# Performance work log

Measured on AMD Instinct MI355X. Metric: run time of the kernel, lower is better.

Reference implementation:

```python
import jax, jax.numpy as jnp
import numpy as np

N, C, H, W = 2, 128, 64, 64
N_HEAD = 4
GROUPS = 16
EPS = 1e-5


def group_norm(x, scale, offset):
    # haiku GroupNorm, channels_first: normalize over (channels-in-group, h, w)
    n, c, h, w = x.shape
    xg = x.reshape(n, GROUPS, c // GROUPS, h, w)
    mu = xg.mean(axis=(2, 3, 4), keepdims=True)
    var = xg.var(axis=(2, 3, 4), keepdims=True)
    xg = (xg - mu) * jax.lax.rsqrt(var + EPS)
    return xg.reshape(n, c, h, w) * scale[None, :, None, None] + offset[None, :, None, None]


def setup_inputs() -> dict:
    key = jax.random.key(0)
    ks = jax.random.split(key, 4)
    inv_sqrt_c = 1.0 / np.sqrt(C).astype(np.float32)
    return {
        "x": jax.random.normal(ks[0], (N, C, H, W), dtype=jnp.float32),
        "w_qkv": jax.random.normal(ks[1], (C, 3 * C), dtype=jnp.float32) * inv_sqrt_c,
        "b_qkv": jnp.zeros((3 * C,), dtype=jnp.float32),
        "w_out": jax.random.normal(ks[2], (C, C), dtype=jnp.float32) * inv_sqrt_c,
        "b_out": jnp.zeros((C,), dtype=jnp.float32),
        "gn1_scale": jnp.ones((C,), dtype=jnp.float32),
        "gn1_offset": jnp.zeros((C,), dtype=jnp.float32),
        "gn2_scale": jnp.ones((C,), dtype=jnp.float32),
        "gn2_offset": jnp.zeros((C,), dtype=jnp.float32),
    }


def reference(x, w_qkv, b_qkv, w_out, b_out, gn1_scale, gn1_offset, gn2_scale, gn2_offset):
    n, c, h, w = x.shape
    dh = c // N_HEAD
    # GroupNorm (x is reassigned, so the residual uses the normalized x)
    xn = group_norm(x, gn1_scale, gn1_offset)
    # 1x1 conv qkv projection: [n, 3c, h, w]
    qkv = jnp.einsum('nchw,cd->ndhw', xn, w_qkv) + b_qkv[None, :, None, None]
    # [n, 3H, dh, hw] -> [n, 3H, hw, dh]
    qkv = jnp.swapaxes(qkv.reshape(n, N_HEAD * 3, dh, h * w), 2, 3)
    q, k, v = jnp.split(qkv, 3, axis=1)  # each [n, H, hw, dh]
    scale = dh ** (-0.25)
    # [n, H, hw, hw] attention matrix (the memory-bound core)
    att = jax.nn.softmax((q * scale) @ (jnp.swapaxes(k, 2, 3) * scale), axis=3)
    y = jnp.swapaxes(att @ v, 2, 3).reshape(n, c, h, w)
    # 1x1 conv out projection + GroupNorm + residual
    out = jnp.einsum('nchw,cd->ndhw', y, w_out) + b_out[None, :, None, None]
    return xn + group_norm(out, gn2_scale, gn2_offset)
```

## Files before the change

### kernel.cpp

```cpp
#include <hip/hip_runtime.h>
#include <hip/hip_bf16.h>
#include <math.h>

constexpr int cHW   = 4096;
constexpr int cC    = 128;
constexpr int cNH   = 4;
constexpr int cDH   = 32;
constexpr float cEPS = 1e-5f;
constexpr float cQS = 0.2550347805f;
constexpr int SPLIT = 4;

typedef short bh8  __attribute__((ext_vector_type(8)));
typedef float f4   __attribute__((ext_vector_type(4)));
typedef float f16a __attribute__((ext_vector_type(16)));

static __device__ __forceinline__ unsigned short f2bf(float f) {
  union { __hip_bfloat16 h; unsigned short u; } cv;
  cv.h = __float2bfloat16(f);
  return cv.u;
}
static __device__ __forceinline__ unsigned pack2bf(float a, float b) {
  return (unsigned)f2bf(a) | ((unsigned)f2bf(b) << 16);
}
static __device__ __forceinline__ unsigned pack_trunc(float a, float b) {
  unsigned ua = __builtin_bit_cast(unsigned, a);
  unsigned ub = __builtin_bit_cast(unsigned, b);
  return (ua >> 16) | (ub & 0xffff0000u);
}
static __device__ __forceinline__ float bflo(unsigned pk) {
  return __builtin_bit_cast(float, pk << 16);
}
static __device__ __forceinline__ float bfhi(unsigned pk) {
  return __builtin_bit_cast(float, pk & 0xffff0000u);
}
static __device__ __forceinline__ void plswap(unsigned& a, unsigned& b) {
#if __has_builtin(__builtin_amdgcn_permlane32_swap)
  typedef int v2i __attribute__((ext_vector_type(2)));
  v2i r = __builtin_amdgcn_permlane32_swap((int)a, (int)b, false, false);
  a = (unsigned)r[0]; b = (unsigned)r[1];
#else
  asm("v_permlane32_swap_b32 %0, %1" : "+v"(a), "+v"(b));
#endif
}
static __device__ __forceinline__ bh8 mk8(unsigned a, unsigned b, unsigned c, unsigned d) {
  union { unsigned u[4]; bh8 v; } t;
  t.u[0] = a; t.u[1] = b; t.u[2] = c; t.u[3] = d;
  return t.v;
}

__device__ __forceinline__ void block_reduce2(float& a, float& b, float* sbuf) {
  #pragma unroll
  for (int off = 32; off > 0; off >>= 1) {
    a += __shfl_down(a, off, 64);
    b += __shfl_down(b, off, 64);
  }
  int wave = threadIdx.x >> 6;
  int lane = threadIdx.x & 63;
  if (lane == 0) { sbuf[wave] = a; sbuf[4 + wave] = b; }
  __syncthreads();
  if (threadIdx.x == 0) {
    sbuf[8] = sbuf[0] + sbuf[1] + sbuf[2] + sbuf[3];
    sbuf[9] = sbuf[4] + sbuf[5] + sbuf[6] + sbuf[7];
  }
  __syncthreads();
  a = sbuf[8];
  b = sbuf[9];
}

__global__ __launch_bounds__(256)
void prep(const float* __restrict__ x, float* __restrict__ part,
          const float* __restrict__ wq, const float* __restrict__ wo,
          unsigned short* __restrict__ wqT, unsigned short* __restrict__ woT) {
  __shared__ float lds[32 * 133];
  int L = threadIdx.x;
  if (blockIdx.x < 256) {
    int ng = blockIdx.x >> 3, sl = blockIdx.x & 7;
    const float4* s4 = (const float4*)x;
    float s = 0.f, s2 = 0.f;
    #pragma unroll
    for (int i = 0; i < 4; i++) {
      int idx = i * 256 + L;
      int c = idx >> 7, tt = idx & 127;
      float4 v = s4[(size_t)(ng * 8 + c) * 1024 + sl * 128 + tt];
      s  += v.x + v.y + v.z + v.w;
      s2 += v.x*v.x + v.y*v.y + v.z*v.z + v.w*v.w;
    }
    block_reduce2(s, s2, lds);
    if (L == 0) { part[blockIdx.x * 2] = s; part[blockIdx.x * 2 + 1] = s2; }
  } else {
    int bx = blockIdx.x - 256;
    const float* src; unsigned short* dst; int W, d0;
    if (bx < 12) { src = wq; dst = wqT; W = 384; d0 = bx * 32; }
    else         { src = wo; dst = woT; W = 128; d0 = (bx - 12) * 32; }
    #pragma unroll
    for (int i = 0; i < 16; i++) {
      int c = i * 8 + (L >> 5), d = L & 31;
      lds[d * 133 + c] = src[(size_t)c * W + d0 + d];
    }
    __syncthreads();
    int d = L >> 3, ch = L & 7, c0 = ch * 16;
    unsigned pk[8];
    #pragma unroll
    for (int j = 0; j < 8; j++)
      pk[j] = pack2bf(lds[d * 133 + c0 + 2 * j], lds[d * 133 + c0 + 2 * j + 1]);
    uint4* d4 = (uint4*)(dst + (size_t)(d0 + d) * 128 + c0);
    d4[0] = make_uint4(pk[0], pk[1], pk[2], pk[3]);
    d4[1] = make_uint4(pk[4], pk[5], pk[6], pk[7]);
  }
}

__global__ __launch_bounds__(256)
void gn_stats(const float* __restrict__ src, float* __restrict__ part) {
  __shared__ float sbuf[10];
  int ng = blockIdx.x >> 3, sl = blockIdx.x & 7;
  const float4* s4 = (const float4*)src;
  float s = 0.f, s2 = 0.f;
  #pragma unroll
  for (int i = 0; i < 4; i++) {
    int idx = i * 256 + threadIdx.x;
    int c = idx >> 7, tt = idx & 127;
    float4 v = s4[(size_t)(ng * 8 + c) * 1024 + sl * 128 + tt];
    s  += v.x + v.y + v.z + v.w;
    s2 += v.x*v.x + v.y*v.y + v.z*v.z + v.w*v.w;
  }
  block_reduce2(s, s2, sbuf);
  if (threadIdx.x == 0) { part[blockIdx.x * 2] = s; part[blockIdx.x * 2 + 1] = s2; }
}

__global__ __launch_bounds__(256)
void gn1_pack(const float* __restrict__ x, const float* __restrict__ part,
              const float* __restrict__ sc, const float* __restrict__ of,
              unsigned short* __restrict__ xnB) {
  int cc = blockIdx.x, ts = blockIdx.y, n = blockIdx.z;
  int ng = n * 16 + cc;
  float s = 0.f, s2 = 0.f;
  #pragma unroll
  for (int p = 0; p < 8; p++) { s += part[(ng*8+p)*2]; s2 += part[(ng*8+p)*2+1]; }
  float mu = s * (1.0f / 32768.0f);
  float rinv = rsqrtf(s2 * (1.0f / 32768.0f) - mu * mu + cEPS);
  int t = ts * 256 + threadIdx.x;
  float v[8];
  #pragma unroll
  for (int j = 0; j < 8; j++) {
    int c = cc * 8 + j;
    float a = rinv * sc[c];
    float bo = of[c] - mu * a;
    v[j] = x[((size_t)n * cC + c) * cHW + t] * a + bo;
  }
  unsigned pk[4];
  #pragma unroll
  for (int j = 0; j < 4; j++) pk[j] = pack2bf(v[2*j], v[2*j+1]);
  ((uint4*)xnB)[(size_t)(n * 16 + cc) * cHW + t] = make_uint4(pk[0], pk[1], pk[2], pk[3]);
}

__global__ __launch_bounds__(256)
void qkv_mfma(const unsigned short* __restrict__ xnB, const unsigned short* __restrict__ wqT,
              const float* __restrict__ bq, unsigned* __restrict__ qF,
              unsigned* __restrict__ kF, unsigned* __restrict__ vF) {
  __shared__ float vbuf[64 * 36];
  const int L = threadIdx.x & 63, w = threadIdx.x >> 6;
  const int c16 = L & 15, q = L >> 4;
  const int t0 = blockIdx.x * 64, dg = blockIdx.y, n = blockIdx.z;
  const int nh = n * 4 + (dg & 3), d0 = dg * 32;
  const f4 zf = {0.f, 0.f, 0.f, 0.f};
  f4 acc0 = zf, acc1 = zf;
  const int trow = t0 + w * 16 + c16;
  #pragma unroll
  for (int ks = 0; ks < 4; ks++) {
    bh8 a  = *(const bh8*)(xnB + ((size_t)(n * 16 + ks * 4 + q) * cHW + trow) * 8);
    bh8 b0 = *(const bh8*)(wqT + (size_t)(d0 + c16) * 128 + ks * 32 + q * 8);
    bh8 b1 = *(const bh8*)(wqT + (size_t)(d0 + 16 + c16) * 128 + ks * 32 + q * 8);
    acc0 = __builtin_amdgcn_mfma_f32_16x16x32_bf16(a, b0, acc0, 0, 0, 0);
    acc1 = __builtin_amdgcn_mfma_f32_16x16x32_bf16(a, b1, acc1, 0, 0, 0);
  }
  const float blo = bq[d0 + c16], bhi = bq[d0 + 16 + c16];
  const float scl = (dg < 4) ? cQS : 1.0f;
  #pragma unroll
  for (int r = 0; r < 4; r++) {
    vbuf[(w * 16 + q * 4 + r) * 36 + c16]      = (acc0[r] + blo) * scl;
    vbuf[(w * 16 + q * 4 + r) * 36 + 16 + c16] = (acc1[r] + bhi) * scl;
  }
  __syncthreads();
  const int tl = threadIdx.x >> 7, fr = (threadIdx.x >> 6) & 1, LL = threadIdx.x & 63;
  const int col = LL & 31, h2 = LL >> 5;
  unsigned pk[4];
  if (dg < 8) {
    const float* src = &vbuf[(tl * 32 + col) * 36 + fr * 16 + h2 * 8];
    #pragma unroll
    for (int jj = 0; jj < 4; jj++) pk[jj] = pack2bf(src[2 * jj], src[2 * jj + 1]);
  } else {
    const float* src = &vbuf[(tl * 32 + fr * 16 + h2 * 8) * 36 + col];
    #pragma unroll
    for (int jj = 0; jj < 4; jj++) pk[jj] = pack2bf(src[2 * jj * 36], src[(2 * jj + 1) * 36]);
  }
  unsigned* dst = (dg < 4) ? qF : ((dg < 8) ? kF : vF);
  size_t frag = ((size_t)(nh * 128 + (t0 >> 5) + tl) * 2 + fr) * 64 + LL;
  ((uint4*)dst)[frag] = make_uint4(pk[0], pk[1], pk[2], pk[3]);
}

__global__ __launch_bounds__(256, 4)
void flash_mfma(const unsigned short* __restrict__ qF,
                const unsigned short* __restrict__ kF,
                const unsigned short* __restrict__ vF,
                unsigned* __restrict__ opart, float* __restrict__ lpart) {
  const int w = threadIdx.x >> 6, L = threadIdx.x & 63;
  const int col = L & 31, hi = L >> 5;
  const int qt = blockIdx.x * 4 + w, nh = blockIdx.y, ph = blockIdx.z;
  const short oneb = 0x3F80;
  const bh8 ones = {oneb, oneb, oneb, oneb, oneb, oneb, oneb, oneb};
  const f16a zf16 = {0.f,0.f,0.f,0.f, 0.f,0.f,0.f,0.f, 0.f,0.f,0.f,0.f, 0.f,0.f,0.f,0.f};

  const unsigned short* qb = qF + ((size_t)(nh * 128 + qt) * 2) * 512;
  bh8 qf0 = *(const bh8*)(qb + L * 8);
  bh8 qf1 = *(const bh8*)(qb + 512 + L * 8);

  const unsigned short* kb = kF + (size_t)nh * 128 * 1024;
  const unsigned short* vb = vF + (size_t)nh * 128 * 1024;

  f16a o = zf16, lacc = zf16;

  const int tb0 = ph * (cHW / SPLIT / 32);
  #pragma unroll 2
  for (int tl = tb0; tl < tb0 + 32; ++tl) {
    const unsigned short* kp = kb + (size_t)tl * 1024;
    const unsigned short* vp = vb + (size_t)tl * 1024;
    bh8 ka0 = *(const bh8*)(kp + L * 8);
    bh8 ka1 = *(const bh8*)(kp + 512 + L * 8);
    bh8 vfa = *(const bh8*)(vp + L * 8);
    bh8 vfb = *(const bh8*)(vp + 512 + L * 8);
    f16a s = __builtin_amdgcn_mfma_f32_32x32x16_bf16(ka0, qf0, zf16, 0, 0, 0);
    s = __builtin_amdgcn_mfma_f32_32x32x16_bf16(ka1, qf1, s, 0, 0, 0);
    #pragma unroll
    for (int r = 0; r < 16; r++) s[r] = __builtin_amdgcn_exp2f(s[r]);
    unsigned pk0 = pack_trunc(s[0],  s[1]);
    unsigned pk1 = pack_trunc(s[2],  s[3]);
    unsigned pk2 = pack_trunc(s[4],  s[5]);
    unsigned pk3 = pack_trunc(s[6],  s[7]);
    unsigned pk4 = pack_trunc(s[8],  s[9]);
    unsigned pk5 = pack_trunc(s[10], s[11]);
    unsigned pk6 = pack_trunc(s[12], s[13]);
    unsigned pk7 = pack_trunc(s[14], s[15]);
    plswap(pk0, pk2); plswap(pk1, pk3);
    plswap(pk4, pk6); plswap(pk5, pk7);
    bh8 pf0 = mk8(pk0, pk1, pk2, pk3);
    bh8 pf1 = mk8(pk4, pk5, pk6, pk7);
    o    = __builtin_amdgcn_mfma_f32_32x32x16_bf16(pf0, vfa,  o,    0, 0, 0);
    lacc = __builtin_amdgcn_mfma_f32_32x32x16_bf16(pf0, ones, lacc, 0, 0, 0);
    o    = __builtin_amdgcn_mfma_f32_32x32x16_bf16(pf1, vfb,  o,    0, 0, 0);
    lacc = __builtin_amdgcn_mfma_f32_32x32x16_bf16(pf1, ones, lacc, 0, 0, 0);
  }

  const size_t base = (size_t)ph * 32768 + (size_t)nh * cHW + (size_t)qt * 32;
  #pragma unroll
  for (int k = 0; k < 8; k++) {
    const int rowlo = ((2 * k) & 3) + 8 * (k >> 1) + 4 * hi;
    opart[((base + rowlo) >> 1) * 32 + col] = pack_trunc(o[2 * k], o[2 * k + 1]);
  }
  if (col == 0) {
    #pragma unroll
    for (int r = 0; r < 16; r++)
      lpart[base + (r & 3) + 8 * (r >> 2) + 4 * hi] = lacc[r];
  }
}

__global__ __launch_bounds__(256)
void combine(const unsigned* __restrict__ opart, const float* __restrict__ lpart,
             unsigned* __restrict__ yB) {
  int tid = blockIdx.x * 256 + threadIdx.x;
  size_t rp = (size_t)(tid >> 1);
  int h = tid & 1;
  size_t r0 = rp * 2;
  float l0 = 0.f, l1 = 0.f;
  #pragma unroll
  for (int p = 0; p < SPLIT; p++) {
    l0 += lpart[(size_t)p * 32768 + r0];
    l1 += lpart[(size_t)p * 32768 + r0 + 1];
  }
  float e0[16], e1[16];
  #pragma unroll
  for (int j = 0; j < 16; j++) { e0[j] = 0.f; e1[j] = 0.f; }
  #pragma unroll
  for (int p = 0; p < SPLIT; p++) {
    const uint4* op = (const uint4*)(opart + ((size_t)p * 16384 + rp) * 32 + h * 16);
    #pragma unroll
    for (int j = 0; j < 4; j++) {
      uint4 v = op[j];
      e0[j*4+0] += bflo(v.x); e1[j*4+0] += bfhi(v.x);
      e0[j*4+1] += bflo(v.y); e1[j*4+1] += bfhi(v.y);
      e0[j*4+2] += bflo(v.z); e1[j*4+2] += bfhi(v.z);
      e0[j*4+3] += bflo(v.w); e1[j*4+3] += bfhi(v.w);
    }
  }
  float i0 = 1.0f / l0, i1 = 1.0f / l1;
  unsigned pkA[8], pkB[8];
  #pragma unroll
  for (int j = 0; j < 8; j++) {
    pkA[j] = pack2bf(e0[2*j] * i0, e0[2*j+1] * i0);
    pkB[j] = pack2bf(e1[2*j] * i1, e1[2*j+1] * i1);
  }
  uint4* dA = (uint4*)(yB + r0 * 16 + h * 8);
  dA[0] = make_uint4(pkA[0], pkA[1], pkA[2], pkA[3]);
  dA[1] = make_uint4(pkA[4], pkA[5], pkA[6], pkA[7]);
  uint4* dB = (uint4*)(yB + (r0 + 1) * 16 + h * 8);
  dB[0] = make_uint4(pkB[0], pkB[1], pkB[2], pkB[3]);
  dB[1] = make_uint4(pkB[4], pkB[5], pkB[6], pkB[7]);
}

__global__ __launch_bounds__(256)
void out_mfma(const unsigned short* __restrict__ yB, const unsigned short* __restrict__ woT,
              const float* __restrict__ bo, float* __restrict__ proj) {
  __shared__ float obuf[64 * 36];
  const int L = threadIdx.x & 63, w = threadIdx.x >> 6;
  const int c16 = L & 15, q = L >> 4;
  const int t0 = blockIdx.x * 64, d0 = blockIdx.y * 32, n = blockIdx.z;
  const f4 zf = {0.f, 0.f, 0.f, 0.f};
  f4 acc0 = zf, acc1 = zf;
  const int trow = t0 + w * 16 + c16;
  #pragma unroll
  for (int h = 0; h < 4; h++) {
    bh8 a  = *(const bh8*)(yB + ((size_t)(n * 4 + h) * cHW + trow) * 32 + q * 8);
    bh8 b0 = *(const bh8*)(woT + (size_t)(d0 + c16) * 128 + h * 32 + q * 8);
    bh8 b1 = *(const bh8*)(woT + (size_t)(d0 + 16 + c16) * 128 + h * 32 + q * 8);
    acc0 = __builtin_amdgcn_mfma_f32_16x16x32_bf16(a, b0, acc0, 0, 0, 0);
    acc1 = __builtin_amdgcn_mfma_f32_16x16x32_bf16(a, b1, acc1, 0, 0, 0);
  }
  float blo = bo[d0 + c16], bhi = bo[d0 + 16 + c16];
  #pragma unroll
  for (int r = 0; r < 4; r++) {
    obuf[(w * 16 + q * 4 + r) * 36 + c16]      = acc0[r] + blo;
    obuf[(w * 16 + q * 4 + r) * 36 + 16 + c16] = acc1[r] + bhi;
  }
  __syncthreads();
  int t16 = threadIdx.x & 15, d8 = (threadIdx.x >> 4) & 15;
  #pragma unroll
  for (int tc = 0; tc < 4; tc++)
    #pragma unroll
    for (int hh = 0; hh < 2; hh++) {
      int d = d8 + hh * 16;
      proj[((size_t)n * cC + d0 + d) * cHW + t0 + tc * 16 + t16] =
          obuf[(tc * 16 + t16) * 36 + d];
    }
}

__global__ __launch_bounds__(256)
void gn2_apply(const float* __restrict__ x, const float* __restrict__ proj,
               const float* __restrict__ p1, const float* __restrict__ p2,
               const float* __restrict__ s1, const float* __restrict__ o1,
               const float* __restrict__ s2, const float* __restrict__ o2,
               float* __restrict__ out) {
  int tid = blockIdx.x * 256 + threadIdx.x;
  int Cg = tid >> 8;
  int n = Cg >> 7, ch = Cg & 127, g = ch >> 3, ng = n * 16 + g;
  float sa = 0.f, sb = 0.f, ta = 0.f, tb = 0.f;
  #pragma unroll
  for (int p = 0; p < 8; p++) {
    sa += p1[(ng*8+p)*2]; sb += p1[(ng*8+p)*2+1];
    ta += p2[(ng*8+p)*2]; tb += p2[(ng*8+p)*2+1];
  }
  float mu1 = sa * (1.0f/32768.0f);
  float ri1 = rsqrtf(sb * (1.0f/32768.0f) - mu1*mu1 + cEPS);
  float a1 = ri1 * s1[ch], b1 = o1[ch] - mu1 * a1;
  float mu2 = ta * (1.0f/32768.0f);
  float ri2 = rsqrtf(tb * (1.0f/32768.0f) - mu2*mu2 + cEPS);
  float a2 = ri2 * s2[ch], b2 = o2[ch] - mu2 * a2;
  const float4* x4 = (const float4*)x;
  const float4* pr4 = (const float4*)proj;
  float4* o4 = (float4*)out;
  #pragma unroll
  for (int i = 0; i < 4; i++) {
    size_t f = (size_t)tid * 4 + i;
    float4 xv = x4[f], pv = pr4[f];
    float4 r;
    r.x = xv.x * a1 + b1 + pv.x * a2 + b2;
    r.y = xv.y * a1 + b1 + pv.y * a2 + b2;
    r.z = xv.z * a1 + b1 + pv.z * a2 + b2;
    r.w = xv.w * a1 + b1 + pv.w * a2 + b2;
    o4[f] = r;
  }
}

extern "C" void kernel_launch(void* const* d_in, const int* in_sizes, int n_in,
                              void* d_out, int out_size, void* d_ws, size_t ws_size,
                              hipStream_t stream) {
  const float* x     = (const float*)d_in[0];
  const float* w_qkv = (const float*)d_in[1];
  const float* b_qkv = (const float*)d_in[2];
  const float* w_out = (const float*)d_in[3];
  const float* b_out = (const float*)d_in[4];
  const float* g1s   = (const float*)d_in[5];
  const float* g1o   = (const float*)d_in[6];
  const float* g2s   = (const float*)d_in[7];
  const float* g2o   = (const float*)d_in[8];
  float* out = (float*)d_out;
  float* ws  = (float*)d_ws;

  const size_t MAP = (size_t)2 * cC * cHW;
  float* proj    = ws;
  float* lpart   = proj + MAP;
  float* stats1  = lpart + (size_t)SPLIT * 32768;
  float* stats2  = stats1 + 512;
  unsigned* opart = (unsigned*)(stats2 + 512);
  unsigned* qF   = opart + (size_t)SPLIT * 32768 * 16;
  unsigned* kF   = qF + MAP / 2;
  unsigned* vF   = kF + MAP / 2;
  unsigned* yB   = vF + MAP / 2;
  unsigned short* xnB = (unsigned short*)(yB + MAP / 2);
  unsigned short* wqT = xnB + MAP;
  unsigned short* woT = wqT + 49152;

  prep      <<<dim3(272),           256, 0, stream>>>(x, stats1, w_qkv, w_out, wqT, woT);
  gn1_pack  <<<dim3(16, 16, 2),     256, 0, stream>>>(x, stats1, g1s, g1o, xnB);
  qkv_mfma  <<<dim3(64, 12, 2),     256, 0, stream>>>(xnB, wqT, b_qkv, qF, kF, vF);
  flash_mfma<<<dim3(32, 8, SPLIT),  256, 0, stream>>>((const unsigned short*)qF,
                                                      (const unsigned short*)kF,
                                                      (const unsigned short*)vF,
                                                      opart, lpart);
  combine   <<<dim3(128),           256, 0, stream>>>(opart, lpart, yB);
  out_mfma  <<<dim3(64, 4, 2),      256, 0, stream>>>((const unsigned short*)yB, woT,
                                                      b_out, proj);
  gn_stats  <<<dim3(256),           256, 0, stream>>>(proj, stats2);
  gn2_apply <<<dim3(256),           256, 0, stream>>>(x, proj, stats1, stats2,
                                                      g1s, g1o, g2s, g2o, out);
}
```

Measured before the change: 130.9 us.

## Fuse split combine, out projection and GN2 stats; raise flash split to 8

Merges the combine, out-projection and GroupNorm-2 statistics kernels into one kernel. It reduces the flash partials directly into LDS A-fragments and accumulates per-group sums with atomics into stats2, which prep now zeroes. This removes two launches and the yB and proj round-trips through global memory for the stats. The flash kernel split is raised from 4 to 8 with a higher occupancy hint to put more blocks in flight. In exchange the partial-output traffic doubles and summation order becomes nondeterministic because of the atomics.

```diff
diff --git a/kernel.cpp b/kernel.cpp
--- a/kernel.cpp
+++ b/kernel.cpp
@@ -8,7 +8,7 @@
 constexpr int cDH   = 32;
 constexpr float cEPS = 1e-5f;
 constexpr float cQS = 0.2550347805f;
-constexpr int SPLIT = 4;
+constexpr int SPLIT = 8;
 
 typedef short bh8  __attribute__((ext_vector_type(8)));
 typedef float f4   __attribute__((ext_vector_type(4)));
@@ -70,7 +70,8 @@
 __global__ __launch_bounds__(256)
 void prep(const float* __restrict__ x, float* __restrict__ part,
           const float* __restrict__ wq, const float* __restrict__ wo,
-          unsigned short* __restrict__ wqT, unsigned short* __restrict__ woT) {
+          unsigned short* __restrict__ wqT, unsigned short* __restrict__ woT,
+          float* __restrict__ stats2) {
   __shared__ float lds[32 * 133];
   int L = threadIdx.x;
   if (blockIdx.x < 256) {
@@ -89,6 +90,7 @@
     if (L == 0) { part[blockIdx.x * 2] = s; part[blockIdx.x * 2 + 1] = s2; }
   } else {
     int bx = blockIdx.x - 256;
+    if (bx == 0 && L < 64) stats2[L] = 0.f;
     const float* src; unsigned short* dst; int W, d0;
     if (bx < 12) { src = wq; dst = wqT; W = 384; d0 = bx * 32; }
     else         { src = wo; dst = woT; W = 128; d0 = (bx - 12) * 32; }
@@ -107,24 +109,6 @@
     d4[0] = make_uint4(pk[0], pk[1], pk[2], pk[3]);
     d4[1] = make_uint4(pk[4], pk[5], pk[6], pk[7]);
   }
-}
-
-__global__ __launch_bounds__(256)
-void gn_stats(const float* __restrict__ src, float* __restrict__ part) {
-  __shared__ float sbuf[10];
-  int ng = blockIdx.x >> 3, sl = blockIdx.x & 7;
-  const float4* s4 = (const float4*)src;
-  float s = 0.f, s2 = 0.f;
-  #pragma unroll
-  for (int i = 0; i < 4; i++) {
-    int idx = i * 256 + threadIdx.x;
-    int c = idx >> 7, tt = idx & 127;
-    float4 v = s4[(size_t)(ng * 8 + c) * 1024 + sl * 128 + tt];
-    s  += v.x + v.y + v.z + v.w;
-    s2 += v.x*v.x + v.y*v.y + v.z*v.z + v.w*v.w;
-  }
-  block_reduce2(s, s2, sbuf);
-  if (threadIdx.x == 0) { part[blockIdx.x * 2] = s; part[blockIdx.x * 2 + 1] = s2; }
 }
 
 __global__ __launch_bounds__(256)
@@ -198,7 +182,7 @@
   ((uint4*)dst)[frag] = make_uint4(pk[0], pk[1], pk[2], pk[3]);
 }
 
-__global__ __launch_bounds__(256, 4)
+__global__ __launch_bounds__(256, 8)
 void flash_mfma(const unsigned short* __restrict__ qF,
                 const unsigned short* __restrict__ kF,
                 const unsigned short* __restrict__ vF,
@@ -221,7 +205,7 @@
 
   const int tb0 = ph * (cHW / SPLIT / 32);
   #pragma unroll 2
-  for (int tl = tb0; tl < tb0 + 32; ++tl) {
+  for (int tl = tb0; tl < tb0 + (cHW / SPLIT / 32); ++tl) {
     const unsigned short* kp = kb + (size_t)tl * 1024;
     const unsigned short* vp = vb + (size_t)tl * 1024;
     bh8 ka0 = *(const bh8*)(kp + L * 8);
@@ -263,83 +247,93 @@
   }
 }
 
-__global__ __launch_bounds__(256)
-void combine(const unsigned* __restrict__ opart, const float* __restrict__ lpart,
-             unsigned* __restrict__ yB) {
-  int tid = blockIdx.x * 256 + threadIdx.x;
-  size_t rp = (size_t)(tid >> 1);
-  int h = tid & 1;
-  size_t r0 = rp * 2;
-  float l0 = 0.f, l1 = 0.f;
-  #pragma unroll
-  for (int p = 0; p < SPLIT; p++) {
-    l0 += lpart[(size_t)p * 32768 + r0];
-    l1 += lpart[(size_t)p * 32768 + r0 + 1];
-  }
-  float e0[16], e1[16];
-  #pragma unroll
-  for (int j = 0; j < 16; j++) { e0[j] = 0.f; e1[j] = 0.f; }
-  #pragma unroll
-  for (int p = 0; p < SPLIT; p++) {
-    const uint4* op = (const uint4*)(opart + ((size_t)p * 16384 + rp) * 32 + h * 16);
-    #pragma unroll
-    for (int j = 0; j < 4; j++) {
-      uint4 v = op[j];
-      e0[j*4+0] += bflo(v.x); e1[j*4+0] += bfhi(v.x);
-      e0[j*4+1] += bflo(v.y); e1[j*4+1] += bfhi(v.y);
-      e0[j*4+2] += bflo(v.z); e1[j*4+2] += bfhi(v.z);
-      e0[j*4+3] += bflo(v.w); e1[j*4+3] += bfhi(v.w);
-    }
-  }
-  float i0 = 1.0f / l0, i1 = 1.0f / l1;
-  unsigned pkA[8], pkB[8];
-  #pragma unroll
-  for (int j = 0; j < 8; j++) {
-    pkA[j] = pack2bf(e0[2*j] * i0, e0[2*j+1] * i0);
-    pkB[j] = pack2bf(e1[2*j] * i1, e1[2*j+1] * i1);
-  }
-  uint4* dA = (uint4*)(yB + r0 * 16 + h * 8);
-  dA[0] = make_uint4(pkA[0], pkA[1], pkA[2], pkA[3]);
-  dA[1] = make_uint4(pkA[4], pkA[5], pkA[6], pkA[7]);
-  uint4* dB = (uint4*)(yB + (r0 + 1) * 16 + h * 8);
-  dB[0] = make_uint4(pkB[0], pkB[1], pkB[2], pkB[3]);
-  dB[1] = make_uint4(pkB[4], pkB[5], pkB[6], pkB[7]);
-}
-
-__global__ __launch_bounds__(256)
-void out_mfma(const unsigned short* __restrict__ yB, const unsigned short* __restrict__ woT,
-              const float* __restrict__ bo, float* __restrict__ proj) {
-  __shared__ float obuf[64 * 36];
+__global__ __launch_bounds__(512)
+void out_fused(const unsigned* __restrict__ opart, const float* __restrict__ lpart,
+               const unsigned short* __restrict__ woT, const float* __restrict__ bo,
+               float* __restrict__ proj, float* __restrict__ stats2) {
+  __shared__ uint4 afbuf[1024];
+  __shared__ float obuf[64 * 136];
   const int L = threadIdx.x & 63, w = threadIdx.x >> 6;
   const int c16 = L & 15, q = L >> 4;
-  const int t0 = blockIdx.x * 64, d0 = blockIdx.y * 32, n = blockIdx.z;
+  const int t0 = blockIdx.x * 64, n = blockIdx.y;
+  const int rg = w >> 1;
+  const int trow = t0 + rg * 16 + c16;
   const f4 zf = {0.f, 0.f, 0.f, 0.f};
-  f4 acc0 = zf, acc1 = zf;
-  const int trow = t0 + w * 16 + c16;
-  #pragma unroll
-  for (int h = 0; h < 4; h++) {
-    bh8 a  = *(const bh8*)(yB + ((size_t)(n * 4 + h) * cHW + trow) * 32 + q * 8);
-    bh8 b0 = *(const bh8*)(woT + (size_t)(d0 + c16) * 128 + h * 32 + q * 8);
-    bh8 b1 = *(const bh8*)(woT + (size_t)(d0 + 16 + c16) * 128 + h * 32 + q * 8);
-    acc0 = __builtin_amdgcn_mfma_f32_16x16x32_bf16(a, b0, acc0, 0, 0, 0);
-    acc1 = __builtin_amdgcn_mfma_f32_16x16x32_bf16(a, b1, acc1, 0, 0, 0);
-  }
-  float blo = bo[d0 + c16], bhi = bo[d0 + 16 + c16];
-  #pragma unroll
-  for (int r = 0; r < 4; r++) {
-    obuf[(w * 16 + q * 4 + r) * 36 + c16]      = acc0[r] + blo;
-    obuf[(w * 16 + q * 4 + r) * 36 + 16 + c16] = acc1[r] + bhi;
+
+  #pragma unroll
+  for (int i = 0; i < 2; i++) {
+    const int h = (w & 1) * 2 + i;
+    const size_t grow = (size_t)(n * 4 + h) * cHW + trow;
+    float l = 0.f;
+    #pragma unroll
+    for (int p = 0; p < SPLIT; p++) l += lpart[(size_t)p * 32768 + grow];
+    const size_t rp = grow >> 1;
+    const int par = c16 & 1;
+    float e[8];
+    #pragma unroll
+    for (int j = 0; j < 8; j++) e[j] = 0.f;
+    #pragma unroll
+    for (int p = 0; p < SPLIT; p++) {
+      const uint4* op = (const uint4*)(opart + ((size_t)p * 16384 + rp) * 32 + q * 8);
+      uint4 v0 = op[0], v1 = op[1];
+      unsigned uu[8] = {v0.x, v0.y, v0.z, v0.w, v1.x, v1.y, v1.z, v1.w};
+      #pragma unroll
+      for (int j = 0; j < 8; j++)
+        e[j] += par ? bfhi(uu[j]) : bflo(uu[j]);
+    }
+    const float inv = 1.0f / l;
+    unsigned pk[4];
+    #pragma unroll
+    for (int jj = 0; jj < 4; jj++)
+      pk[jj] = pack2bf(e[2 * jj] * inv, e[2 * jj + 1] * inv);
+    afbuf[(rg * 4 + h) * 64 + L] = make_uint4(pk[0], pk[1], pk[2], pk[3]);
   }
   __syncthreads();
-  int t16 = threadIdx.x & 15, d8 = (threadIdx.x >> 4) & 15;
-  #pragma unroll
-  for (int tc = 0; tc < 4; tc++)
-    #pragma unroll
-    for (int hh = 0; hh < 2; hh++) {
-      int d = d8 + hh * 16;
-      proj[((size_t)n * cC + d0 + d) * cHW + t0 + tc * 16 + t16] =
-          obuf[(tc * 16 + t16) * 36 + d];
-    }
+
+  #pragma unroll
+  for (int i = 0; i < 2; i++) {
+    const int dg = (w & 1) * 2 + i;
+    const int d0 = dg * 32;
+    f4 acc0 = zf, acc1 = zf;
+    #pragma unroll
+    for (int h = 0; h < 4; h++) {
+      bh8 a  = *(const bh8*)&afbuf[(rg * 4 + h) * 64 + L];
+      bh8 b0 = *(const bh8*)(woT + (size_t)(d0 + c16) * 128 + h * 32 + q * 8);
+      bh8 b1 = *(const bh8*)(woT + (size_t)(d0 + 16 + c16) * 128 + h * 32 + q * 8);
+      acc0 = __builtin_amdgcn_mfma_f32_16x16x32_bf16(a, b0, acc0, 0, 0, 0);
+      acc1 = __builtin_amdgcn_mfma_f32_16x16x32_bf16(a, b1, acc1, 0, 0, 0);
+    }
+    const float blo = bo[d0 + c16], bhi = bo[d0 + 16 + c16];
+    #pragma unroll
+    for (int r = 0; r < 4; r++) {
+      obuf[(rg * 16 + q * 4 + r) * 136 + d0 + c16]      = acc0[r] + blo;
+      obuf[(rg * 16 + q * 4 + r) * 136 + d0 + 16 + c16] = acc1[r] + bhi;
+    }
+  }
+  __syncthreads();
+
+  const int t16 = threadIdx.x & 15, dd = threadIdx.x >> 4;
+  float s = 0.f, s2 = 0.f;
+  #pragma unroll
+  for (int jd = 0; jd < 4; jd++) {
+    const int d = dd * 4 + jd;
+    #pragma unroll
+    for (int tc = 0; tc < 4; tc++) {
+      float v = obuf[(tc * 16 + t16) * 136 + d];
+      proj[((size_t)n * cC + d) * cHW + t0 + tc * 16 + t16] = v;
+      s += v; s2 += v * v;
+    }
+  }
+  #pragma unroll
+  for (int off = 16; off > 0; off >>= 1) {
+    s  += __shfl_down(s, off, 32);
+    s2 += __shfl_down(s2, off, 32);
+  }
+  if ((threadIdx.x & 31) == 0) {
+    const int g = threadIdx.x >> 5;
+    atomicAdd(&stats2[n * 32 + g * 2],     s);
+    atomicAdd(&stats2[n * 32 + g * 2 + 1], s2);
+  }
 }
 
 __global__ __launch_bounds__(256)
@@ -351,12 +345,12 @@
   int tid = blockIdx.x * 256 + threadIdx.x;
   int Cg = tid >> 8;
   int n = Cg >> 7, ch = Cg & 127, g = ch >> 3, ng = n * 16 + g;
-  float sa = 0.f, sb = 0.f, ta = 0.f, tb = 0.f;
+  float sa = 0.f, sb = 0.f;
   #pragma unroll
   for (int p = 0; p < 8; p++) {
     sa += p1[(ng*8+p)*2]; sb += p1[(ng*8+p)*2+1];
-    ta += p2[(ng*8+p)*2]; tb += p2[(ng*8+p)*2+1];
-  }
+  }
+  float ta = p2[ng * 2], tb = p2[ng * 2 + 1];
   float mu1 = sa * (1.0f/32768.0f);
   float ri1 = rsqrtf(sb * (1.0f/32768.0f) - mu1*mu1 + cEPS);
   float a1 = ri1 * s1[ch], b1 = o1[ch] - mu1 * a1;
@@ -403,22 +397,20 @@
   unsigned* qF   = opart + (size_t)SPLIT * 32768 * 16;
   unsigned* kF   = qF + MAP / 2;
   unsigned* vF   = kF + MAP / 2;
-  unsigned* yB   = vF + MAP / 2;
-  unsigned short* xnB = (unsigned short*)(yB + MAP / 2);
+  unsigned short* xnB = (unsigned short*)(vF + MAP / 2);
   unsigned short* wqT = xnB + MAP;
   unsigned short* woT = wqT + 49152;
 
-  prep      <<<dim3(272),           256, 0, stream>>>(x, stats1, w_qkv, w_out, wqT, woT);
+  prep      <<<dim3(272),           256, 0, stream>>>(x, stats1, w_qkv, w_out, wqT, woT,
+                                                      stats2);
   gn1_pack  <<<dim3(16, 16, 2),     256, 0, stream>>>(x, stats1, g1s, g1o, xnB);
   qkv_mfma  <<<dim3(64, 12, 2),     256, 0, stream>>>(xnB, wqT, b_qkv, qF, kF, vF);
   flash_mfma<<<dim3(32, 8, SPLIT),  256, 0, stream>>>((const unsigned short*)qF,
                                                       (const unsigned short*)kF,
                                                       (const unsigned short*)vF,
                                                       opart, lpart);
-  combine   <<<dim3(128),           256, 0, stream>>>(opart, lpart, yB);
-  out_mfma  <<<dim3(64, 4, 2),      256, 0, stream>>>((const unsigned short*)yB, woT,
-                                                      b_out, proj);
-  gn_stats  <<<dim3(256),           256, 0, stream>>>(proj, stats2);
+  out_fused <<<dim3(64, 2),         512, 0, stream>>>(opart, lpart, woT, b_out,
+                                                      proj, stats2);
   gn2_apply <<<dim3(256),           256, 0, stream>>>(x, proj, stats1, stats2,
                                                       g1s, g1o, g2s, g2o, out);
 }
```

Result: slower. 329.8 us (+151.8%).
